# Kernel tuning notes

Measured on AMD Instinct MI355X. Metric: run time of the kernel, lower is better.

## Reference

```python
import jax, jax.numpy as jnp
import numpy as np
import math

B, S, DQ, DK, DV, H = 8, 2048, 256, 256, 256, 4
DH = DV // H
EPS = 1e-5

def _layernorm(x, g, b):
    mu = jnp.mean(x, axis=-1, keepdims=True)
    var = jnp.mean(jnp.square(x - mu), axis=-1, keepdims=True)
    return (x - mu) * jax.lax.rsqrt(var + EPS) * g + b

def setup_inputs() -> dict:
    key = jax.random.key(0)
    ks = jax.random.split(key, 12)
    s_in = 1.0 / math.sqrt(DQ)
    s_v = 1.0 / math.sqrt(DV)
    return {
        "Q": jax.random.normal(ks[0], (B, S, DQ), dtype=jnp.float32),
        "K": jax.random.normal(ks[1], (B, S, DK), dtype=jnp.float32),
        "Wq": jax.random.uniform(ks[2], (DQ, DV), jnp.float32, -s_in, s_in),
        "bq": jax.random.uniform(ks[3], (DV,), jnp.float32, -s_in, s_in),
        "Wk": jax.random.uniform(ks[4], (DK, DV), jnp.float32, -s_in, s_in),
        "bk": jax.random.uniform(ks[5], (DV,), jnp.float32, -s_in, s_in),
        "Wv": jax.random.uniform(ks[6], (DK, DV), jnp.float32, -s_in, s_in),
        "bv": jax.random.uniform(ks[7], (DV,), jnp.float32, -s_in, s_in),
        "Wo": jax.random.uniform(ks[8], (DV, DV), jnp.float32, -s_v, s_v),
        "bo": jax.random.uniform(ks[9], (DV,), jnp.float32, -s_v, s_v),
        "g0": jnp.ones((DV,), jnp.float32),
        "beta0": jnp.zeros((DV,), jnp.float32),
        "g1": jnp.ones((DV,), jnp.float32),
        "beta1": jnp.zeros((DV,), jnp.float32),
    }

def reference(Q, K, Wq, bq, Wk, bk, Wv, bv, Wo, bo, g0, beta0, g1, beta1):
    q = Q @ Wq + bq                    # [B,S,DV]
    k = K @ Wk + bk
    v = K @ Wv + bv
    q4 = q.reshape(B, S, H, DH)
    k4 = k.reshape(B, S, H, DH)
    v4 = v.reshape(B, S, H, DH)
    scores = jnp.einsum('bqhd,bkhd->bhqk', q4, k4) / math.sqrt(DH)
    A = jax.nn.softmax(scores, axis=-1)
    o = q4 + jnp.einsum('bhqk,bkhd->bqhd', A, v4)  # residual with projected Q per head
    O = o.reshape(B, S, DV)
    O = _layernorm(O, g0, beta0)
    O = O + jax.nn.relu(O @ Wo + bo)
    O = _layernorm(O, g1, beta1)
    return O
```

## Files before the change

kernel.cpp:

```cpp
#include <hip/hip_runtime.h>
#include <hip/hip_bf16.h>
#include <stdint.h>

typedef uint16_t u16;
typedef uint32_t u32;
typedef __attribute__((ext_vector_type(8))) short short8;
typedef __attribute__((ext_vector_type(4))) float f32x4;

#define LOG2E 1.44269504088896340736f

__device__ __forceinline__ u16 f2bf(float f) {
    u32 u = __builtin_bit_cast(u32, f);
    return (u16)((u + 0x7fffu + ((u >> 16) & 1u)) >> 16);
}
__device__ __forceinline__ float bf2f(u16 h) {
    u32 u = ((u32)h) << 16;
    return __builtin_bit_cast(float, u);
}
__device__ __forceinline__ u32 pack_bf16(float lo, float hi) {
    return (u32)f2bf(lo) | ((u32)f2bf(hi) << 16);
}
__device__ __forceinline__ u32 pack_bf16_fast(float lo, float hi) {
    u32 a = __builtin_bit_cast(u32, lo) + 0x8000u;
    u32 b = __builtin_bit_cast(u32, hi) + 0x8000u;
    return (a >> 16) | (b & 0xffff0000u);
}

__global__ void wt_kernel(const float* __restrict__ Wq, const float* __restrict__ Wk,
                          const float* __restrict__ Wv, const float* __restrict__ Wo,
                          const float* __restrict__ bk, u16* __restrict__ WT,
                          float* __restrict__ bks) {
    const int wsel = blockIdx.y, k = blockIdx.x, n = threadIdx.x;
    const float* W = (wsel == 0) ? Wq : (wsel == 1) ? Wk : (wsel == 2) ? Wv : Wo;
    const float scale = (wsel == 1) ? (0.125f * LOG2E) : 1.0f;
    WT[(size_t)wsel * 65536 + (size_t)n * 256 + k] = f2bf(W[(size_t)k * 256 + n] * scale);
    if (wsel == 1 && k == 0) bks[n] = bk[n] * (0.125f * LOG2E);
}

__global__ __launch_bounds__(256)
void proj_kernel(const float* __restrict__ Qf, const float* __restrict__ Kf,
                 const u16* __restrict__ WT, const float* __restrict__ bq,
                 const float* __restrict__ bks, const float* __restrict__ bvv,
                 u16* __restrict__ qb, u16* __restrict__ kbuf, u16* __restrict__ vbuf) {
    const int z = blockIdx.z;
    const float* Af = (z == 0) ? Qf : Kf;
    const u16* BT = WT + z * 65536;
    const float* bias = (z == 0) ? bq : (z == 1) ? bks : bvv;
    u16* out = (z == 0) ? qb : (z == 1) ? kbuf : vbuf;

    __shared__ u16 As[128 * 64];
    __shared__ u16 Bs[128 * 64];
    const int tid = threadIdx.x;
    const int w = tid >> 6, lane = tid & 63;
    const int g = lane >> 4, lo = lane & 15;
    const int rowB = blockIdx.x * 128;
    const int colB = blockIdx.y * 128;
    const int wr = (w >> 1) * 64, wc = (w & 1) * 64;

    const f32x4 fz = {0.f, 0.f, 0.f, 0.f};
    f32x4 acc[4][4];
#pragma unroll
    for (int m = 0; m < 4; ++m)
#pragma unroll
        for (int n = 0; n < 4; ++n) acc[m][n] = fz;

    const int srow = tid & 127;
    const int shalf = tid >> 7;

#pragma unroll 1
    for (int kt = 0; kt < 4; ++kt) {
        const int k0 = kt * 64;
        __syncthreads();
        {
            const float* ga = Af + (size_t)(rowB + srow) * 256 + k0 + shalf * 32;
            uint4 pa[4];
#pragma unroll
            for (int j = 0; j < 4; ++j) {
                float4 x = *(const float4*)(ga + j * 8);
                float4 y = *(const float4*)(ga + j * 8 + 4);
                pa[j].x = pack_bf16(x.x, x.y);
                pa[j].y = pack_bf16(x.z, x.w);
                pa[j].z = pack_bf16(y.x, y.y);
                pa[j].w = pack_bf16(y.z, y.w);
            }
            const u16* gb = BT + (size_t)(colB + srow) * 256 + k0 + shalf * 32;
            uint4 b0 = *(const uint4*)gb;
            uint4 b1 = *(const uint4*)(gb + 8);
            uint4 b2 = *(const uint4*)(gb + 16);
            uint4 b3 = *(const uint4*)(gb + 24);
            const u32 sw = (u32)((srow & 7) << 4);
            const u32 ba = (u32)(srow * 128 + shalf * 64);
            *(uint4*)((char*)As + ((ba) ^ sw))      = pa[0];
            *(uint4*)((char*)As + ((ba + 16) ^ sw)) = pa[1];
            *(uint4*)((char*)As + ((ba + 32) ^ sw)) = pa[2];
            *(uint4*)((char*)As + ((ba + 48) ^ sw)) = pa[3];
            *(uint4*)((char*)Bs + ((ba) ^ sw))      = b0;
            *(uint4*)((char*)Bs + ((ba + 16) ^ sw)) = b1;
            *(uint4*)((char*)Bs + ((ba + 32) ^ sw)) = b2;
            *(uint4*)((char*)Bs + ((ba + 48) ^ sw)) = b3;
        }
        __syncthreads();
#pragma unroll
        for (int c = 0; c < 2; ++c) {
            short8 af[4], bfr[4];
#pragma unroll
            for (int m = 0; m < 4; ++m) {
                const int row = wr + m * 16 + lo;
                const u32 addr = (u32)(row * 128 + c * 64 + g * 16) ^ (u32)((row & 7) << 4);
                af[m] = *(const short8*)((char*)As + addr);
            }
#pragma unroll
            for (int n = 0; n < 4; ++n) {
                const int row = wc + n * 16 + lo;
                const u32 addr = (u32)(row * 128 + c * 64 + g * 16) ^ (u32)((row & 7) << 4);
                bfr[n] = *(const short8*)((char*)Bs + addr);
            }
#pragma unroll
            for (int m = 0; m < 4; ++m)
#pragma unroll
                for (int n = 0; n < 4; ++n)
                    acc[m][n] = __builtin_amdgcn_mfma_f32_16x16x32_bf16(af[m], bfr[n], acc[m][n], 0, 0, 0);
        }
    }

    float bv[4];
#pragma unroll
    for (int n = 0; n < 4; ++n) bv[n] = bias[colB + wc + n * 16 + lo];
#pragma unroll
    for (int m = 0; m < 4; ++m)
#pragma unroll
        for (int r = 0; r < 4; ++r) {
            const size_t row = (size_t)(rowB + wr + m * 16 + g * 4 + r);
#pragma unroll
            for (int n = 0; n < 4; ++n)
                out[row * 256 + colB + wc + n * 16 + lo] = f2bf(acc[m][n][r] + bv[n]);
        }
}

__global__ __launch_bounds__(512, 4)
void attn_kernel(const u16* __restrict__ qb, const u16* __restrict__ kb,
                 const u16* __restrict__ vb, u16* __restrict__ Ob) {
    __shared__ u16 Klds[2 * 64 * 64];
    __shared__ u16 Vtlds[2 * 64 * 64];
    __shared__ u16 Plds[8 * 16 * 64];
    const int tid = threadIdx.x;
    const int w = tid >> 6, lane = tid & 63;
    const int g = lane >> 4, lo = lane & 15;
    const int bid = blockIdx.x;
    const int xcd = bid & 7;
    const int member = (bid >> 3) & 15;
    const int grp = ((bid >> 7) << 3) | xcd;
    const int q0 = member * 128;
    const int h = grp & 3, b = grp >> 2;
    const size_t hbase = (size_t)b * 2048 * 256 + (size_t)h * 64;

    short8 qf[2];
#pragma unroll
    for (int c = 0; c < 2; ++c) {
        const size_t row = (size_t)(q0 + w * 16 + lo);
        qf[c] = *(const short8*)&qb[hbase + row * 256 + c * 32 + g * 8];
    }
    const short8 vones = {0x3F80, 0x3F80, 0x3F80, 0x3F80, 0x3F80, 0x3F80, 0x3F80, 0x3F80};

    const f32x4 fz = {0.f, 0.f, 0.f, 0.f};
    f32x4 oacc[4];
#pragma unroll
    for (int n = 0; n < 4; ++n) oacc[n] = fz;
    f32x4 l_acc = fz;
    float m_run = -1e30f;

    char* Pb = (char*)Plds + w * 2048;

    const bool kRole = (tid < 256);
    const int skey = tid & 63, sseg = (tid >> 6) & 3;
    const int t4 = tid & 255;
    const int vkey = (t4 & 31) * 2, vd0 = (t4 >> 5) * 8;
    const u16* gbase;
    int goff2;
    if (kRole) { gbase = &kb[hbase + (size_t)skey * 256 + sseg * 16]; goff2 = 8; }
    else       { gbase = &vb[hbase + (size_t)vkey * 256 + vd0];       goff2 = 256; }

    uint4 s0, s1;
    auto load_tile = [&](int kt) {
        const u16* p = gbase + (size_t)kt * 16384;
        s0 = *(const uint4*)p;
        s1 = *(const uint4*)(p + goff2);
    };
    auto write_tile = [&](int sel) {
        if (kRole) {
            char* Kb_ = (char*)Klds + sel * 8192;
            const u32 sw = (u32)((skey & 7) << 4);
            const u32 ba = (u32)(skey * 128 + sseg * 32);
            *(uint4*)(Kb_ + ((ba) ^ sw)) = s0;
            *(uint4*)(Kb_ + ((ba + 16) ^ sw)) = s1;
        } else {
            char* Vb_ = (char*)Vtlds + sel * 8192;
            union { uint4 v; u16 hh[8]; } a0, a1;
            a0.v = s0; a1.v = s1;
#pragma unroll
            for (int i = 0; i < 8; ++i) {
                const int d = vd0 + i;
                const u32 addr = (u32)(d * 128 + vkey * 2) ^ (u32)((d & 7) << 4);
                *(u32*)(Vb_ + addr) = (u32)a0.hh[i] | ((u32)a1.hh[i] << 16);
            }
        }
    };

    load_tile(0);
    write_tile(0);
    load_tile(1);
    __syncthreads();

#pragma unroll 1
    for (int kt = 0; kt < 32; ++kt) {
        const int cur = kt & 1;
        char* Klb = (char*)Klds + cur * 8192;
        char* Vtb = (char*)Vtlds + cur * 8192;

        f32x4 sc[4];
#pragma unroll
        for (int km = 0; km < 4; ++km) sc[km] = fz;
        __builtin_amdgcn_s_setprio(1);
#pragma unroll
        for (int c = 0; c < 2; ++c)
#pragma unroll
            for (int km = 0; km < 4; ++km) {
                const int key = km * 16 + lo;
                const u32 addr = (u32)(key * 128 + c * 64 + g * 16) ^ (u32)((key & 7) << 4);
                const short8 kf = *(const short8*)(Klb + addr);
                sc[km] = __builtin_amdgcn_mfma_f32_16x16x32_bf16(kf, qf[c], sc[km], 0, 0, 0);
            }
        __builtin_amdgcn_s_setprio(0);

        float mt = -1e30f;
#pragma unroll
        for (int km = 0; km < 4; ++km)
#pragma unroll
            for (int r = 0; r < 4; ++r) mt = fmaxf(mt, sc[km][r]);
        mt = fmaxf(mt, __shfl_xor(mt, 16));
        mt = fmaxf(mt, __shfl_xor(mt, 32));
        if (!__all(mt <= m_run + 11.5f)) {
            const float mnew = fmaxf(m_run, mt);
            const float alpha = __builtin_amdgcn_exp2f(m_run - mnew);
#pragma unroll
            for (int r = 0; r < 4; ++r) {
                const float a = __shfl(alpha, (lane & 48) | (g * 4 + r));
                l_acc[r] *= a;
#pragma unroll
                for (int n = 0; n < 4; ++n) oacc[n][r] *= a;
            }
            m_run = mnew;
        }
#pragma unroll
        for (int km = 0; km < 4; ++km)
#pragma unroll
            for (int r = 0; r < 4; ++r)
                sc[km][r] = __builtin_amdgcn_exp2f(sc[km][r] - m_run);

        {
            const u32 sw = (u32)((lo & 7) << 4);
#pragma unroll
            for (int km = 0; km < 4; ++km) {
                uint2 val;
                val.x = pack_bf16_fast(sc[km][0], sc[km][1]);
                val.y = pack_bf16_fast(sc[km][2], sc[km][3]);
                const u32 addr = (u32)(lo * 128 + km * 32 + g * 8) ^ sw;
                *(uint2*)(Pb + addr) = val;
            }
        }

        __builtin_amdgcn_s_setprio(1);
#pragma unroll
        for (int c = 0; c < 2; ++c) {
            const u32 paddr = (u32)(lo * 128 + c * 64 + g * 16) ^ (u32)((lo & 7) << 4);
            const short8 pf = *(const short8*)(Pb + paddr);
#pragma unroll
            for (int n = 0; n < 4; ++n) {
                const int d = n * 16 + lo;
                const u32 addr = (u32)(d * 128 + c * 64 + g * 16) ^ (u32)((d & 7) << 4);
                const short8 vf = *(const short8*)(Vtb + addr);
                oacc[n] = __builtin_amdgcn_mfma_f32_16x16x32_bf16(pf, vf, oacc[n], 0, 0, 0);
            }
            l_acc = __builtin_amdgcn_mfma_f32_16x16x32_bf16(pf, vones, l_acc, 0, 0, 0);
        }
        __builtin_amdgcn_s_setprio(0);

        if (kt < 31) write_tile(cur ^ 1);
        if (kt < 30) load_tile(kt + 2);
        __syncthreads();
    }

#pragma unroll
    for (int r = 0; r < 4; ++r) {
        const float li = 1.0f / l_acc[r];
        const size_t row = (size_t)(q0 + w * 16 + g * 4 + r);
#pragma unroll
        for (int n = 0; n < 4; ++n) {
            const int d = n * 16 + lo;
            const size_t idx = hbase + row * 256 + d;
            Ob[idx] = f2bf(oacc[n][r] * li + bf2f(qb[idx]));
        }
    }
}

__global__ __launch_bounds__(256)
void ln0_kernel(const u16* in, const float* __restrict__ gam,
                const float* __restrict__ bet, float* __restrict__ of,
                u16* ob) {
    const int w = threadIdx.x >> 6, lane = threadIdx.x & 63;
    const size_t row = (size_t)blockIdx.x * 4 + w;
    const uint2 raw = *(const uint2*)(in + row * 256 + lane * 4);
    float4 v;
    v.x = bf2f((u16)(raw.x & 0xffff));
    v.y = bf2f((u16)(raw.x >> 16));
    v.z = bf2f((u16)(raw.y & 0xffff));
    v.w = bf2f((u16)(raw.y >> 16));
    float s = v.x + v.y + v.z + v.w;
    float q = v.x * v.x + v.y * v.y + v.z * v.z + v.w * v.w;
#pragma unroll
    for (int m = 1; m <= 32; m <<= 1) {
        s += __shfl_xor(s, m);
        q += __shfl_xor(q, m);
    }
    const float mu = s * (1.f / 256.f);
    const float var = q * (1.f / 256.f) - mu * mu;
    const float rstd = rsqrtf(var + 1e-5f);
    const float4 gv = ((const float4*)gam)[lane];
    const float4 bv = ((const float4*)bet)[lane];
    float4 y;
    y.x = (v.x - mu) * rstd * gv.x + bv.x;
    y.y = (v.y - mu) * rstd * gv.y + bv.y;
    y.z = (v.z - mu) * rstd * gv.z + bv.z;
    y.w = (v.w - mu) * rstd * gv.w + bv.w;
    ((float4*)(of + row * 256))[lane] = y;
    uint2 pk;
    pk.x = pack_bf16(y.x, y.y);
    pk.y = pack_bf16(y.z, y.w);
    *(uint2*)(ob + row * 256 + lane * 4) = pk;
}

__global__ __launch_bounds__(256)
void mlp_ln1_kernel(const u16* __restrict__ A, const u16* __restrict__ BT,
                    const float* __restrict__ bias, const float* __restrict__ gam,
                    const float* __restrict__ bet, float* out) {
    __shared__ char lds[40960];
    u16* As = (u16*)lds;
    u16* Bs = (u16*)(lds + 8192);
    char* Ys = lds;
    const int tid = threadIdx.x;
    const int w = tid >> 6, lane = tid & 63;
    const int g = lane >> 4, lo = lane & 15;
    const int rowB = blockIdx.x * 64;
    const int wc = w * 64;

    const f32x4 fz = {0.f, 0.f, 0.f, 0.f};
    f32x4 acc[4][4];
#pragma unroll
    for (int m = 0; m < 4; ++m)
#pragma unroll
        for (int n = 0; n < 4; ++n) acc[m][n] = fz;

    const int arow = tid & 63, aqtr = tid >> 6;
#pragma unroll 1
    for (int kt = 0; kt < 4; ++kt) {
        const int k0 = kt * 64;
        __syncthreads();
        {
            const u16* ga = A + (size_t)(rowB + arow) * 256 + k0 + aqtr * 16;
            uint4 a0 = *(const uint4*)ga;
            uint4 a1 = *(const uint4*)(ga + 8);
            const u32 swA = (u32)((arow & 7) << 4);
            const u32 baA = (u32)(arow * 128 + aqtr * 32);
            *(uint4*)((char*)As + ((baA) ^ swA))      = a0;
            *(uint4*)((char*)As + ((baA + 16) ^ swA)) = a1;
            const u16* gb = BT + (size_t)tid * 256 + k0;
            const u32 swB = (u32)((tid & 7) << 4);
            const u32 baB = (u32)(tid * 128);
#pragma unroll
            for (int j = 0; j < 8; ++j) {
                uint4 bj = *(const uint4*)(gb + j * 8);
                *(uint4*)((char*)Bs + ((baB + j * 16) ^ swB)) = bj;
            }
        }
        __syncthreads();
#pragma unroll
        for (int c = 0; c < 2; ++c) {
            short8 af[4], bfr[4];
#pragma unroll
            for (int m = 0; m < 4; ++m) {
                const int row = m * 16 + lo;
                const u32 addr = (u32)(row * 128 + c * 64 + g * 16) ^ (u32)((row & 7) << 4);
                af[m] = *(const short8*)((char*)As + addr);
            }
#pragma unroll
            for (int n = 0; n < 4; ++n) {
                const int row = wc + n * 16 + lo;
                const u32 addr = (u32)(row * 128 + c * 64 + g * 16) ^ (u32)((row & 7) << 4);
                bfr[n] = *(const short8*)((char*)Bs + addr);
            }
#pragma unroll
            for (int m = 0; m < 4; ++m)
#pragma unroll
                for (int n = 0; n < 4; ++n)
                    acc[m][n] = __builtin_amdgcn_mfma_f32_16x16x32_bf16(af[m], bfr[n], acc[m][n], 0, 0, 0);
        }
    }

    float bv[4];
#pragma unroll
    for (int n = 0; n < 4; ++n) bv[n] = bias[wc + n * 16 + lo];

    __syncthreads();

#pragma unroll
    for (int m = 0; m < 4; ++m)
#pragma unroll
        for (int r = 0; r < 4; ++r) {
            const int row_l = m * 16 + g * 4 + r;
            const u32 sw = (u32)((row_l & 7) << 4);
            const size_t grow = (size_t)(rowB + row_l);
#pragma unroll
            for (int n = 0; n < 4; ++n) {
                const int col = wc + n * 16 + lo;
                const float y = out[grow * 256 + col] + fmaxf(acc[m][n][r] + bv[n], 0.f);
                const u32 badr = (u32)(row_l * 512 + col * 2);
                const u32 addr = (badr & ~15u) ^ sw;
                *(u16*)(Ys + addr + (badr & 15u)) = f2bf(y);
            }
        }
    __syncthreads();

    {
        const int row = tid >> 2, qtr = tid & 3;
        const u32 sw = (u32)((row & 7) << 4);
        const u32 rbase = (u32)(row * 512 + qtr * 128);
        float s = 0.f, q = 0.f;
#pragma unroll
        for (int j = 0; j < 8; ++j) {
            uint4 v4 = *(const uint4*)(Ys + ((rbase + j * 16) ^ sw));
            const u32 uu[4] = {v4.x, v4.y, v4.z, v4.w};
#pragma unroll
            for (int e = 0; e < 4; ++e) {
                const float f0 = bf2f((u16)(uu[e] & 0xffff));
                const float f1 = bf2f((u16)(uu[e] >> 16));
                s += f0 + f1;
                q += f0 * f0 + f1 * f1;
            }
        }
        s += __shfl_xor(s, 1); q += __shfl_xor(q, 1);
        s += __shfl_xor(s, 2); q += __shfl_xor(q, 2);
        const float mu = s * (1.f / 256.f);
        const float var = q * (1.f / 256.f) - mu * mu;
        const float rstd = rsqrtf(var + 1e-5f);
        const size_t grow = (size_t)(rowB + row);
        float* op = out + grow * 256 + qtr * 64;
        const float* gp = gam + qtr * 64;
        const float* bp = bet + qtr * 64;
#pragma unroll
        for (int j = 0; j < 8; ++j) {
            uint4 v4 = *(const uint4*)(Ys + ((rbase + j * 16) ^ sw));
            const u32 uu[4] = {v4.x, v4.y, v4.z, v4.w};
#pragma unroll
            for (int e = 0; e < 2; ++e) {
                float4 gv = *(const float4*)(gp + j * 8 + e * 4);
                float4 bb = *(const float4*)(bp + j * 8 + e * 4);
                float4 o4;
                o4.x = (bf2f((u16)(uu[e * 2]     & 0xffff)) - mu) * rstd * gv.x + bb.x;
                o4.y = (bf2f((u16)(uu[e * 2]     >> 16))    - mu) * rstd * gv.y + bb.y;
                o4.z = (bf2f((u16)(uu[e * 2 + 1] & 0xffff)) - mu) * rstd * gv.z + bb.z;
                o4.w = (bf2f((u16)(uu[e * 2 + 1] >> 16))    - mu) * rstd * gv.w + bb.w;
                *(float4*)(op + j * 8 + e * 4) = o4;
            }
        }
    }
}

extern "C" void kernel_launch(void* const* d_in, const int* in_sizes, int n_in,
                              void* d_out, int out_size, void* d_ws, size_t ws_size,
                              hipStream_t stream) {
    const float* Q  = (const float*)d_in[0];
    const float* K  = (const float*)d_in[1];
    const float* Wq = (const float*)d_in[2];
    const float* bq = (const float*)d_in[3];
    const float* Wk = (const float*)d_in[4];
    const float* bk = (const float*)d_in[5];
    const float* Wv = (const float*)d_in[6];
    const float* bv = (const float*)d_in[7];
    const float* Wo = (const float*)d_in[8];
    const float* bo = (const float*)d_in[9];
    const float* g0 = (const float*)d_in[10];
    const float* be0 = (const float*)d_in[11];
    const float* g1 = (const float*)d_in[12];
    const float* be1 = (const float*)d_in[13];
    float* out = (float*)d_out;

    const size_t NE = (size_t)8 * 2048 * 256;
    char* ws = (char*)d_ws;
    size_t off = 0;
    auto alloc = [&](size_t bytes) { char* p = ws + off; off += (bytes + 255) & ~(size_t)255; return p; };
    u16* qb   = (u16*)alloc(NE * 2);
    u16* kbuf = (u16*)alloc(NE * 2);
    u16* vbuf = (u16*)alloc(NE * 2);
    u16* WT   = (u16*)alloc(4 * 65536 * 2);
    float* bks = (float*)alloc(256 * 4);
    u16* Ob16 = (u16*)alloc(NE * 2);

    wt_kernel<<<dim3(256, 4), 256, 0, stream>>>(Wq, Wk, Wv, Wo, bk, WT, bks);

    proj_kernel<<<dim3(128, 2, 3), 256, 0, stream>>>(Q, K, WT, bq, bks, bv, qb, kbuf, vbuf);

    attn_kernel<<<512, 512, 0, stream>>>(qb, kbuf, vbuf, Ob16);

    ln0_kernel<<<4096, 256, 0, stream>>>(Ob16, g0, be0, out, Ob16);

    mlp_ln1_kernel<<<256, 256, 0, stream>>>(Ob16, WT + 3 * 65536, bo, g1, be1, out);
}
```

Measured before the change: 125.7 us.

## Fuse LayerNorm0 into MLP tail kernel and retile projection GEMM to full-width columns

Merges the first LayerNorm into the Wo-MLP/LayerNorm1 kernel. The normalized rows are kept as bf16 in shared memory and serve both as the GEMM A operand and as the residual, so the fp32 round-trip through the output buffer and one launch are removed. The residual now comes from bf16 instead of fp32, which adds a small extra rounding. The projection GEMM is retiled from 128x128 to 64x256 tiles (768 blocks), so each A row is loaded and converted once instead of twice. This costs fewer rows per block and a larger B tile in shared memory.

```diff
diff --git a/kernel.cpp b/kernel.cpp
--- a/kernel.cpp
+++ b/kernel.cpp
@@ -42,20 +42,19 @@
                  const u16* __restrict__ WT, const float* __restrict__ bq,
                  const float* __restrict__ bks, const float* __restrict__ bvv,
                  u16* __restrict__ qb, u16* __restrict__ kbuf, u16* __restrict__ vbuf) {
-    const int z = blockIdx.z;
+    const int z = blockIdx.y;
     const float* Af = (z == 0) ? Qf : Kf;
     const u16* BT = WT + z * 65536;
     const float* bias = (z == 0) ? bq : (z == 1) ? bks : bvv;
     u16* out = (z == 0) ? qb : (z == 1) ? kbuf : vbuf;
 
-    __shared__ u16 As[128 * 64];
-    __shared__ u16 Bs[128 * 64];
+    __shared__ u16 As[64 * 64];
+    __shared__ u16 Bs[256 * 64];
     const int tid = threadIdx.x;
     const int w = tid >> 6, lane = tid & 63;
     const int g = lane >> 4, lo = lane & 15;
-    const int rowB = blockIdx.x * 128;
-    const int colB = blockIdx.y * 128;
-    const int wr = (w >> 1) * 64, wc = (w & 1) * 64;
+    const int rowB = blockIdx.x * 64;
+    const int wc = w * 64;
 
     const f32x4 fz = {0.f, 0.f, 0.f, 0.f};
     f32x4 acc[4][4];
@@ -64,40 +63,35 @@
 #pragma unroll
         for (int n = 0; n < 4; ++n) acc[m][n] = fz;
 
-    const int srow = tid & 127;
-    const int shalf = tid >> 7;
+    const int arow = tid & 63, aqtr = tid >> 6;
 
 #pragma unroll 1
     for (int kt = 0; kt < 4; ++kt) {
         const int k0 = kt * 64;
         __syncthreads();
         {
-            const float* ga = Af + (size_t)(rowB + srow) * 256 + k0 + shalf * 32;
-            uint4 pa[4];
-#pragma unroll
-            for (int j = 0; j < 4; ++j) {
-                float4 x = *(const float4*)(ga + j * 8);
-                float4 y = *(const float4*)(ga + j * 8 + 4);
-                pa[j].x = pack_bf16(x.x, x.y);
-                pa[j].y = pack_bf16(x.z, x.w);
-                pa[j].z = pack_bf16(y.x, y.y);
-                pa[j].w = pack_bf16(y.z, y.w);
-            }
-            const u16* gb = BT + (size_t)(colB + srow) * 256 + k0 + shalf * 32;
-            uint4 b0 = *(const uint4*)gb;
-            uint4 b1 = *(const uint4*)(gb + 8);
-            uint4 b2 = *(const uint4*)(gb + 16);
-            uint4 b3 = *(const uint4*)(gb + 24);
-            const u32 sw = (u32)((srow & 7) << 4);
-            const u32 ba = (u32)(srow * 128 + shalf * 64);
-            *(uint4*)((char*)As + ((ba) ^ sw))      = pa[0];
-            *(uint4*)((char*)As + ((ba + 16) ^ sw)) = pa[1];
-            *(uint4*)((char*)As + ((ba + 32) ^ sw)) = pa[2];
-            *(uint4*)((char*)As + ((ba + 48) ^ sw)) = pa[3];
-            *(uint4*)((char*)Bs + ((ba) ^ sw))      = b0;
-            *(uint4*)((char*)Bs + ((ba + 16) ^ sw)) = b1;
-            *(uint4*)((char*)Bs + ((ba + 32) ^ sw)) = b2;
-            *(uint4*)((char*)Bs + ((ba + 48) ^ sw)) = b3;
+            const float* ga = Af + (size_t)(rowB + arow) * 256 + k0 + aqtr * 16;
+            float4 x0 = *(const float4*)ga;
+            float4 x1 = *(const float4*)(ga + 4);
+            float4 x2 = *(const float4*)(ga + 8);
+            float4 x3 = *(const float4*)(ga + 12);
+            uint4 pa0, pa1;
+            pa0.x = pack_bf16(x0.x, x0.y); pa0.y = pack_bf16(x0.z, x0.w);
+            pa0.z = pack_bf16(x1.x, x1.y); pa0.w = pack_bf16(x1.z, x1.w);
+            pa1.x = pack_bf16(x2.x, x2.y); pa1.y = pack_bf16(x2.z, x2.w);
+            pa1.z = pack_bf16(x3.x, x3.y); pa1.w = pack_bf16(x3.z, x3.w);
+            const u32 swA = (u32)((arow & 7) << 4);
+            const u32 baA = (u32)(arow * 128 + aqtr * 32);
+            *(uint4*)((char*)As + ((baA) ^ swA))      = pa0;
+            *(uint4*)((char*)As + ((baA + 16) ^ swA)) = pa1;
+            const u16* gb = BT + (size_t)tid * 256 + k0;
+            const u32 swB = (u32)((tid & 7) << 4);
+            const u32 baB = (u32)(tid * 128);
+#pragma unroll
+            for (int j = 0; j < 8; ++j) {
+                uint4 bj = *(const uint4*)(gb + j * 8);
+                *(uint4*)((char*)Bs + ((baB + j * 16) ^ swB)) = bj;
+            }
         }
         __syncthreads();
 #pragma unroll
@@ -105,7 +99,7 @@
             short8 af[4], bfr[4];
 #pragma unroll
             for (int m = 0; m < 4; ++m) {
-                const int row = wr + m * 16 + lo;
+                const int row = m * 16 + lo;
                 const u32 addr = (u32)(row * 128 + c * 64 + g * 16) ^ (u32)((row & 7) << 4);
                 af[m] = *(const short8*)((char*)As + addr);
             }
@@ -125,15 +119,15 @@
 
     float bv[4];
 #pragma unroll
-    for (int n = 0; n < 4; ++n) bv[n] = bias[colB + wc + n * 16 + lo];
+    for (int n = 0; n < 4; ++n) bv[n] = bias[wc + n * 16 + lo];
 #pragma unroll
     for (int m = 0; m < 4; ++m)
 #pragma unroll
         for (int r = 0; r < 4; ++r) {
-            const size_t row = (size_t)(rowB + wr + m * 16 + g * 4 + r);
+            const size_t row = (size_t)(rowB + m * 16 + g * 4 + r);
 #pragma unroll
             for (int n = 0; n < 4; ++n)
-                out[row * 256 + colB + wc + n * 16 + lo] = f2bf(acc[m][n][r] + bv[n]);
+                out[row * 256 + wc + n * 16 + lo] = f2bf(acc[m][n][r] + bv[n]);
         }
 }
 
@@ -304,55 +298,68 @@
 }
 
 __global__ __launch_bounds__(256)
-void ln0_kernel(const u16* in, const float* __restrict__ gam,
-                const float* __restrict__ bet, float* __restrict__ of,
-                u16* ob) {
-    const int w = threadIdx.x >> 6, lane = threadIdx.x & 63;
-    const size_t row = (size_t)blockIdx.x * 4 + w;
-    const uint2 raw = *(const uint2*)(in + row * 256 + lane * 4);
-    float4 v;
-    v.x = bf2f((u16)(raw.x & 0xffff));
-    v.y = bf2f((u16)(raw.x >> 16));
-    v.z = bf2f((u16)(raw.y & 0xffff));
-    v.w = bf2f((u16)(raw.y >> 16));
-    float s = v.x + v.y + v.z + v.w;
-    float q = v.x * v.x + v.y * v.y + v.z * v.z + v.w * v.w;
-#pragma unroll
-    for (int m = 1; m <= 32; m <<= 1) {
-        s += __shfl_xor(s, m);
-        q += __shfl_xor(q, m);
-    }
-    const float mu = s * (1.f / 256.f);
-    const float var = q * (1.f / 256.f) - mu * mu;
-    const float rstd = rsqrtf(var + 1e-5f);
-    const float4 gv = ((const float4*)gam)[lane];
-    const float4 bv = ((const float4*)bet)[lane];
-    float4 y;
-    y.x = (v.x - mu) * rstd * gv.x + bv.x;
-    y.y = (v.y - mu) * rstd * gv.y + bv.y;
-    y.z = (v.z - mu) * rstd * gv.z + bv.z;
-    y.w = (v.w - mu) * rstd * gv.w + bv.w;
-    ((float4*)(of + row * 256))[lane] = y;
-    uint2 pk;
-    pk.x = pack_bf16(y.x, y.y);
-    pk.y = pack_bf16(y.z, y.w);
-    *(uint2*)(ob + row * 256 + lane * 4) = pk;
-}
-
-__global__ __launch_bounds__(256)
-void mlp_ln1_kernel(const u16* __restrict__ A, const u16* __restrict__ BT,
-                    const float* __restrict__ bias, const float* __restrict__ gam,
-                    const float* __restrict__ bet, float* out) {
-    __shared__ char lds[40960];
-    u16* As = (u16*)lds;
-    u16* Bs = (u16*)(lds + 8192);
-    char* Ys = lds;
+void tail_kernel(const u16* __restrict__ Ob, const u16* __restrict__ BT,
+                 const float* __restrict__ bo, const float* __restrict__ g0,
+                 const float* __restrict__ be0, const float* __restrict__ g1,
+                 const float* __restrict__ be1, float* __restrict__ out) {
+    __shared__ char lds[65536];
+    char* Xs = lds;
+    u16* Bs = (u16*)(lds + 32768);
     const int tid = threadIdx.x;
     const int w = tid >> 6, lane = tid & 63;
     const int g = lane >> 4, lo = lane & 15;
     const int rowB = blockIdx.x * 64;
     const int wc = w * 64;
 
+    {
+        const int row = tid >> 2, qtr = tid & 3;
+        const size_t grow = (size_t)(rowB + row);
+        const u16* src = Ob + grow * 256 + qtr * 64;
+        uint4 r8[8];
+#pragma unroll
+        for (int j = 0; j < 8; ++j) r8[j] = *(const uint4*)(src + j * 8);
+        float s = 0.f, q = 0.f;
+#pragma unroll
+        for (int j = 0; j < 8; ++j) {
+            const u32 uu[4] = {r8[j].x, r8[j].y, r8[j].z, r8[j].w};
+#pragma unroll
+            for (int e = 0; e < 4; ++e) {
+                const float f0 = bf2f((u16)(uu[e] & 0xffff));
+                const float f1 = bf2f((u16)(uu[e] >> 16));
+                s += f0 + f1;
+                q += f0 * f0 + f1 * f1;
+            }
+        }
+        s += __shfl_xor(s, 1); q += __shfl_xor(q, 1);
+        s += __shfl_xor(s, 2); q += __shfl_xor(q, 2);
+        const float mu = s * (1.f / 256.f);
+        const float var = q * (1.f / 256.f) - mu * mu;
+        const float rstd = rsqrtf(var + 1e-5f);
+        const u32 sw = (u32)((row & 7) << 4);
+        const float* gp = g0 + qtr * 64;
+        const float* bp = be0 + qtr * 64;
+#pragma unroll
+        for (int j = 0; j < 8; ++j) {
+            const u32 uu[4] = {r8[j].x, r8[j].y, r8[j].z, r8[j].w};
+            float4 gv0 = *(const float4*)(gp + j * 8);
+            float4 gv1 = *(const float4*)(gp + j * 8 + 4);
+            float4 bb0 = *(const float4*)(bp + j * 8);
+            float4 bb1 = *(const float4*)(bp + j * 8 + 4);
+            uint4 o;
+            o.x = pack_bf16((bf2f((u16)(uu[0] & 0xffff)) - mu) * rstd * gv0.x + bb0.x,
+                            (bf2f((u16)(uu[0] >> 16))    - mu) * rstd * gv0.y + bb0.y);
+            o.y = pack_bf16((bf2f((u16)(uu[1] & 0xffff)) - mu) * rstd * gv0.z + bb0.z,
+                            (bf2f((u16)(uu[1] >> 16))    - mu) * rstd * gv0.w + bb0.w);
+            o.z = pack_bf16((bf2f((u16)(uu[2] & 0xffff)) - mu) * rstd * gv1.x + bb1.x,
+                            (bf2f((u16)(uu[2] >> 16))    - mu) * rstd * gv1.y + bb1.y);
+            o.w = pack_bf16((bf2f((u16)(uu[3] & 0xffff)) - mu) * rstd * gv1.z + bb1.z,
+                            (bf2f((u16)(uu[3] >> 16))    - mu) * rstd * gv1.w + bb1.w);
+            const u32 addr = (u32)(row * 512 + qtr * 128 + j * 16) ^ sw;
+            *(uint4*)(Xs + addr) = o;
+        }
+    }
+    __syncthreads();
+
     const f32x4 fz = {0.f, 0.f, 0.f, 0.f};
     f32x4 acc[4][4];
 #pragma unroll
@@ -360,19 +367,11 @@
 #pragma unroll
         for (int n = 0; n < 4; ++n) acc[m][n] = fz;
 
-    const int arow = tid & 63, aqtr = tid >> 6;
 #pragma unroll 1
     for (int kt = 0; kt < 4; ++kt) {
         const int k0 = kt * 64;
-        __syncthreads();
+        if (kt) __syncthreads();
         {
-            const u16* ga = A + (size_t)(rowB + arow) * 256 + k0 + aqtr * 16;
-            uint4 a0 = *(const uint4*)ga;
-            uint4 a1 = *(const uint4*)(ga + 8);
-            const u32 swA = (u32)((arow & 7) << 4);
-            const u32 baA = (u32)(arow * 128 + aqtr * 32);
-            *(uint4*)((char*)As + ((baA) ^ swA))      = a0;
-            *(uint4*)((char*)As + ((baA + 16) ^ swA)) = a1;
             const u16* gb = BT + (size_t)tid * 256 + k0;
             const u32 swB = (u32)((tid & 7) << 4);
             const u32 baB = (u32)(tid * 128);
@@ -389,8 +388,8 @@
 #pragma unroll
             for (int m = 0; m < 4; ++m) {
                 const int row = m * 16 + lo;
-                const u32 addr = (u32)(row * 128 + c * 64 + g * 16) ^ (u32)((row & 7) << 4);
-                af[m] = *(const short8*)((char*)As + addr);
+                const u32 addr = (u32)(row * 512 + kt * 128 + c * 64 + g * 16) ^ (u32)((row & 7) << 4);
+                af[m] = *(const short8*)(Xs + addr);
             }
 #pragma unroll
             for (int n = 0; n < 4; ++n) {
@@ -408,7 +407,7 @@
 
     float bv[4];
 #pragma unroll
-    for (int n = 0; n < 4; ++n) bv[n] = bias[wc + n * 16 + lo];
+    for (int n = 0; n < 4; ++n) bv[n] = bo[wc + n * 16 + lo];
 
     __syncthreads();
 
@@ -418,14 +417,13 @@
         for (int r = 0; r < 4; ++r) {
             const int row_l = m * 16 + g * 4 + r;
             const u32 sw = (u32)((row_l & 7) << 4);
-            const size_t grow = (size_t)(rowB + row_l);
 #pragma unroll
             for (int n = 0; n < 4; ++n) {
                 const int col = wc + n * 16 + lo;
-                const float y = out[grow * 256 + col] + fmaxf(acc[m][n][r] + bv[n], 0.f);
                 const u32 badr = (u32)(row_l * 512 + col * 2);
-                const u32 addr = (badr & ~15u) ^ sw;
-                *(u16*)(Ys + addr + (badr & 15u)) = f2bf(y);
+                char* p = Xs + ((badr & ~15u) ^ sw) + (badr & 15u);
+                const float resid = bf2f(*(u16*)p);
+                *(u16*)p = f2bf(resid + fmaxf(acc[m][n][r] + bv[n], 0.f));
             }
         }
     __syncthreads();
@@ -437,7 +435,7 @@
         float s = 0.f, q = 0.f;
 #pragma unroll
         for (int j = 0; j < 8; ++j) {
-            uint4 v4 = *(const uint4*)(Ys + ((rbase + j * 16) ^ sw));
+            uint4 v4 = *(const uint4*)(Xs + ((rbase + j * 16) ^ sw));
             const u32 uu[4] = {v4.x, v4.y, v4.z, v4.w};
 #pragma unroll
             for (int e = 0; e < 4; ++e) {
@@ -454,11 +452,11 @@
         const float rstd = rsqrtf(var + 1e-5f);
         const size_t grow = (size_t)(rowB + row);
         float* op = out + grow * 256 + qtr * 64;
-        const float* gp = gam + qtr * 64;
-        const float* bp = bet + qtr * 64;
+        const float* gp = g1 + qtr * 64;
+        const float* bp = be1 + qtr * 64;
 #pragma unroll
         for (int j = 0; j < 8; ++j) {
-            uint4 v4 = *(const uint4*)(Ys + ((rbase + j * 16) ^ sw));
+            uint4 v4 = *(const uint4*)(Xs + ((rbase + j * 16) ^ sw));
             const u32 uu[4] = {v4.x, v4.y, v4.z, v4.w};
 #pragma unroll
             for (int e = 0; e < 2; ++e) {
@@ -507,11 +505,9 @@
 
     wt_kernel<<<dim3(256, 4), 256, 0, stream>>>(Wq, Wk, Wv, Wo, bk, WT, bks);
 
-    proj_kernel<<<dim3(128, 2, 3), 256, 0, stream>>>(Q, K, WT, bq, bks, bv, qb, kbuf, vbuf);
+    proj_kernel<<<dim3(256, 3), 256, 0, stream>>>(Q, K, WT, bq, bks, bv, qb, kbuf, vbuf);
 
     attn_kernel<<<512, 512, 0, stream>>>(qb, kbuf, vbuf, Ob16);
 
-    ln0_kernel<<<4096, 256, 0, stream>>>(Ob16, g0, be0, out, Ob16);
-
-    mlp_ln1_kernel<<<256, 256, 0, stream>>>(Ob16, WT + 3 * 65536, bo, g1, be1, out);
-}
+    tail_kernel<<<256, 256, 0, stream>>>(Ob16, WT + 3 * 65536, bo, g0, be0, g1, be1, out);
+}
```

After: 120.8 us. 1.04x faster.
